# Kernel tuning notes

Measured on AMD Instinct MI355X. Metric: run time of the kernel, lower is better.

Reference implementation:

```python
import jax, jax.numpy as jnp
import numpy as np

NEG_SLOPE = 0.2
EPS = 1e-16


def setup_inputs() -> dict:
    N, E, IN, H, C = 100000, 1600000, 128, 4, 16
    key = jax.random.key(0)
    k1, k2, k3, k4, k5 = jax.random.split(key, 5)
    x = jax.random.normal(k1, (N, IN), dtype=jnp.float32)
    edge_index = jax.random.randint(k2, (2, E), 0, N, dtype=jnp.int64)
    # Xavier-uniform init like nn.init.xavier_uniform_
    limW = float(np.sqrt(6.0 / (IN + H * C)))
    W = jax.random.uniform(k3, (IN, H * C), dtype=jnp.float32, minval=-limW, maxval=limW)
    lima = float(np.sqrt(6.0 / (H + C)))
    att = jax.random.uniform(k4, (1, H, C), dtype=jnp.float32, minval=-lima, maxval=lima)
    bias = jnp.zeros((H * C,), dtype=jnp.float32)
    return {"x": x, "edge_index": edge_index, "W": W, "att": att, "bias": bias}


def reference(x, edge_index, W, att, bias):
    N = x.shape[0]
    H, C = att.shape[1], att.shape[2]
    h = (x @ W).reshape(N, H, C)  # [N,H,C]
    # add self loops
    loops = jnp.arange(N, dtype=edge_index.dtype)
    row = jnp.concatenate([edge_index[0], loops])  # target nodes
    col = jnp.concatenate([edge_index[1], loops])  # source nodes
    x_i = h[row]  # [Etot,H,C]
    x_j = h[col]
    e = jax.nn.leaky_relu(x_i + x_j, NEG_SLOPE)
    alpha = jnp.einsum('ehc,hc->eh', e, att[0])  # [Etot,H]
    # segment softmax keyed by row (every node has a self loop -> no empty segments)
    amax = jax.lax.stop_gradient(jax.ops.segment_max(alpha, row, num_segments=N))
    ea = jnp.exp(alpha - amax[row])
    denom = jax.ops.segment_sum(ea, row, num_segments=N)
    alpha = ea / (denom[row] + EPS)
    # weighted message scatter-add (dropout p=0 / eval mode)
    out = jax.ops.segment_sum(x_j * alpha[:, :, None], row, num_segments=N)  # [N,H,C]
    out = out.reshape(N, H * C) + bias  # concat=True
    return out
```

## Files before the change

### kernel.cpp

```cpp
#include <hip/hip_runtime.h>

#define NEG_SLOPE 0.2f

typedef float f32x4 __attribute__((ext_vector_type(4)));
typedef short bf16x8 __attribute__((ext_vector_type(8)));

__device__ __forceinline__ unsigned short f2bf(float f) {
  union { float f; unsigned u; } v; v.f = f;
  unsigned r = v.u + 0x7fff + ((v.u >> 16) & 1);
  return (unsigned short)(r >> 16);
}
__device__ __forceinline__ float bf2f(unsigned short u) {
  union { unsigned u; float f; } v; v.u = ((unsigned)u) << 16;
  return v.f;
}
__device__ __forceinline__ unsigned pkbf(float a, float b) {
  return (unsigned)f2bf(a) | ((unsigned)f2bf(b) << 16);
}
__device__ __forceinline__ f32x4 upk4(unsigned ux, unsigned uy) {
  union { unsigned u; float f; } a, b, c, d;
  a.u = ux << 16; b.u = ux & 0xffff0000u;
  c.u = uy << 16; d.u = uy & 0xffff0000u;
  f32x4 r; r.x = a.f; r.y = b.f; r.z = c.f; r.w = d.f;
  return r;
}
__device__ __forceinline__ f32x4 absfma(f32x4 s, f32x4 coef, f32x4 d) {
  d.x = fmaf(fabsf(s.x), coef.x, d.x);
  d.y = fmaf(fabsf(s.y), coef.y, d.y);
  d.z = fmaf(fabsf(s.z), coef.z, d.z);
  d.w = fmaf(fabsf(s.w), coef.w, d.w);
  return d;
}
__device__ __forceinline__ float dpp_xor1_add(float x) {
  int y = __builtin_amdgcn_mov_dpp(__builtin_bit_cast(int, x), 0xB1, 0xF, 0xF, true);
  return x + __builtin_bit_cast(float, y);
}
__device__ __forceinline__ float dpp_xor2_add(float x) {
  int y = __builtin_amdgcn_mov_dpp(__builtin_bit_cast(int, x), 0x4E, 0xF, 0xF, true);
  return x + __builtin_bit_cast(float, y);
}

#define TILE 4096
#define EPT 16
#define NBKT_MAX 256
#define SMEM_BYTES 24576

__device__ __forceinline__ void gemm_role(const float* __restrict__ x,
                                          const float* __restrict__ W,
                                          unsigned short* __restrict__ hb, int N,
                                          char* smem, int bid) {
  uint4* Bl = (uint4*)smem;
  const int t = threadIdx.x;
  {
    const int l = t & 63;
    const int kt = (t >> 6) & 3;
    const int kb = kt * 32 + ((l >> 4) * 8);
    const int cb = l & 15;
#pragma unroll
    for (int ct = 0; ct < 4; ct++) {
      const float* wp = W + (size_t)kb * 64 + ct * 16 + cb;
      unsigned p[4];
#pragma unroll
      for (int jj = 0; jj < 4; jj++)
        p[jj] = pkbf(wp[(2 * jj) * 64], wp[(2 * jj + 1) * 64]);
      Bl[(ct * 4 + kt) * 64 + l] = make_uint4(p[0], p[1], p[2], p[3]);
    }
  }
  __syncthreads();
  const int l = t & 63;
  const int wv = t >> 6;
  union BU { bf16x8 v; uint4 q; };
  BU b[4][4];
#pragma unroll
  for (int ct = 0; ct < 4; ct++)
#pragma unroll
    for (int kt = 0; kt < 4; kt++) b[ct][kt].q = Bl[(ct * 4 + kt) * 64 + l];

  const int rowbase0 = bid * 256 + wv * 64;
#pragma unroll
  for (int rt = 0; rt < 4; rt++) {
    const int rbase = rowbase0 + rt * 16;
    int rl = rbase + (l & 15);
    if (rl >= N) rl = N - 1;
    const float* xp = x + (size_t)rl * 128 + ((l >> 4) * 8);
    BU ah[4], alo[4];
#pragma unroll
    for (int kt = 0; kt < 4; kt++) {
      float f[8];
      float4 v0 = *(const float4*)(xp + kt * 32);
      float4 v1 = *(const float4*)(xp + kt * 32 + 4);
      f[0] = v0.x; f[1] = v0.y; f[2] = v0.z; f[3] = v0.w;
      f[4] = v1.x; f[5] = v1.y; f[6] = v1.z; f[7] = v1.w;
      unsigned short hs[8], ls[8];
#pragma unroll
      for (int j = 0; j < 8; j++) {
        hs[j] = f2bf(f[j]);
        ls[j] = f2bf(f[j] - bf2f(hs[j]));
      }
      ah[kt].q = make_uint4(hs[0] | (hs[1] << 16), hs[2] | (hs[3] << 16),
                            hs[4] | (hs[5] << 16), hs[6] | (hs[7] << 16));
      alo[kt].q = make_uint4(ls[0] | (ls[1] << 16), ls[2] | (ls[3] << 16),
                             ls[4] | (ls[5] << 16), ls[6] | (ls[7] << 16));
    }
#pragma unroll
    for (int ct = 0; ct < 4; ct++) {
      f32x4 acc = {0.f, 0.f, 0.f, 0.f};
#pragma unroll
      for (int kt = 0; kt < 4; kt++) {
        acc = __builtin_amdgcn_mfma_f32_16x16x32_bf16(ah[kt].v, b[ct][kt].v, acc, 0, 0, 0);
        acc = __builtin_amdgcn_mfma_f32_16x16x32_bf16(alo[kt].v, b[ct][kt].v, acc, 0, 0, 0);
      }
#pragma unroll
      for (int j = 0; j < 4; j++) {
        float v = acc[j];
        float pv = __shfl_xor(v, 1);
        int row = rbase + (l >> 4) * 4 + j;
        if (!(l & 1) && row < N) {
          *(unsigned*)((char*)hb + (size_t)row * 128 + ct * 32 + (l & 15) * 2) =
              pkbf(v, pv);
        }
      }
    }
  }
}

__device__ __forceinline__ void bucket_role(const int* __restrict__ rowi,
                                            const int* __restrict__ coli,
                                            int* __restrict__ bucket_fill,
                                            unsigned* __restrict__ bucket_arr, int E,
                                            int Cedge, int Ctot, int NBKT, char* smem,
                                            int bid) {
  int* cnt = (int*)smem;
  int* gadj = cnt + 256;
  int* tmp = gadj + 256;
  unsigned* staged = (unsigned*)(tmp + 256);
  unsigned char* bkof = (unsigned char*)(staged + TILE);
  const int t = threadIdx.x;
  const int tile0 = bid * TILE;
  const int nt = min(TILE, E - tile0);
  cnt[t] = 0;
  __syncthreads();
  unsigned pk[EPT];
  int bk[EPT];
#pragma unroll
  for (int j = 0; j < EPT; j++) {
    int i = tile0 + j * 256 + t;
    if (i < E) {
      int r = rowi[i];
      int c = coli[i];
      bk[j] = r >> 9;
      pk[j] = ((unsigned)(r & 511) << 17) | (unsigned)c;
      atomicAdd(&cnt[bk[j]], 1);
    } else {
      bk[j] = -1;
    }
  }
  __syncthreads();
  int v = cnt[t];
  tmp[t] = v;
  __syncthreads();
  for (int off = 1; off < 256; off <<= 1) {
    int val = tmp[t] + ((t >= off) ? tmp[t - off] : 0);
    __syncthreads();
    tmp[t] = val;
    __syncthreads();
  }
  int ex = tmp[t] - v;
  int ga = 0;
  if (v > 0) ga = atomicAdd(&bucket_fill[t], v);
  gadj[t] = ga - ex;
  cnt[t] = ex;
  __syncthreads();
#pragma unroll
  for (int j = 0; j < EPT; j++) {
    if (bk[j] >= 0) {
      int lp = atomicAdd(&cnt[bk[j]], 1);
      staged[lp] = pk[j];
      bkof[lp] = (unsigned char)bk[j];
    }
  }
  __syncthreads();
  for (int i = t; i < nt; i += 256) {
    int b = bkof[i];
    int pb = i + gadj[b];
    if (pb < Cedge) bucket_arr[b * Ctot + pb] = staged[i];
  }
}

__global__ __launch_bounds__(256) void gemm_bucket(const float* __restrict__ x,
                                                   const float* __restrict__ W,
                                                   unsigned short* __restrict__ hb, int N,
                                                   const int* __restrict__ rowi,
                                                   const int* __restrict__ coli,
                                                   int* __restrict__ bucket_fill,
                                                   unsigned* __restrict__ bucket_arr,
                                                   int E, int Cedge, int Ctot, int NBKT,
                                                   int G1) {
  __shared__ __align__(16) char smem[SMEM_BYTES];
  if ((int)blockIdx.x < G1)
    gemm_role(x, W, hb, N, smem, blockIdx.x);
  else
    bucket_role(rowi, coli, bucket_fill, bucket_arr, E, Cedge, Ctot, NBKT, smem,
                blockIdx.x - G1);
}

#define STAGE_CAP 10240

__global__ __launch_bounds__(1024) void csr_pass(unsigned* __restrict__ bucket_arr,
                                                 const int* __restrict__ bucket_fill,
                                                 int2* __restrict__ rowinfo,
                                                 int Cedge, int Ctot, int N) {
  __shared__ unsigned stage[STAGE_CAP];
  __shared__ int hist[512], excl[512], pairs[256];
  const int t = threadIdx.x;
  const int b = blockIdx.x;
  const int bb = b * Ctot;
  const int r0 = b << 9;
  const int nb = min(bucket_fill[b], Cedge);
  for (int i = t; i < 512; i += 1024) hist[i] = ((r0 + i) < N) ? 1 : 0;
  for (int i = t; i < nb; i += 1024) stage[i] = bucket_arr[bb + i];
  __syncthreads();
  for (int i = t; i < nb; i += 1024) atomicAdd(&hist[stage[i] >> 17], 1);
  __syncthreads();
  int h0 = 0, h1 = 0, ps = 0;
  if (t < 256) {
    h0 = hist[2 * t];
    h1 = hist[2 * t + 1];
    ps = h0 + h1;
    pairs[t] = ps;
  }
  __syncthreads();
  for (int off = 1; off < 256; off <<= 1) {
    int val = 0;
    if (t < 256) val = pairs[t] + ((t >= off) ? pairs[t - off] : 0);
    __syncthreads();
    if (t < 256) pairs[t] = val;
    __syncthreads();
  }
  if (t < 256) {
    int pexcl = pairs[t] - ps;
    excl[2 * t] = pexcl;
    excl[2 * t + 1] = pexcl + h0;
  }
  __syncthreads();
  for (int r = t; r < 512; r += 1024) {
    int gr = r0 + r;
    if (gr < N) {
      int o = bb + excl[r];
      rowinfo[gr] = make_int2(o, o + hist[r]);
    }
  }
  __syncthreads();
  for (int i = t; i < nb; i += 1024) {
    unsigned pk = stage[i];
    int r = pk >> 17;
    int lp = atomicAdd(&excl[r], 1);
    bucket_arr[bb + lp] = (pk & 0x1FFFFu) << 7;
  }
  __syncthreads();
  for (int r = t; r < 512; r += 1024) {
    int gr = r0 + r;
    if (gr < N) bucket_arr[bb + excl[r]] = (unsigned)gr << 7;
  }
}

#define ESTEPN(hivX, accX, denX, u)                     \
  {                                                     \
    f32x4 jv = upk4((u).x, (u).y);                      \
    f32x4 s = hivX + jv;                                \
    f32x4 d = s * attA;                                 \
    d = absfma(s, attB, d);                             \
    float al = (d.x + d.y) + (d.z + d.w);               \
    al = dpp_xor1_add(al);                              \
    al = dpp_xor2_add(al);                              \
    float p = exp2f(al);                                \
    accX += jv * p;                                     \
    denX += p;                                          \
  }

__global__ __launch_bounds__(256) void node_pass(const unsigned short* __restrict__ hb,
                                                 const int2* __restrict__ rowinfo,
                                                 const unsigned* __restrict__ srcs,
                                                 const float* __restrict__ att,
                                                 const float* __restrict__ bias,
                                                 float* __restrict__ out, int N) {
  const int wp = (blockIdx.x * blockDim.x + threadIdx.x) >> 6;
  const int a = wp * 2;
  if (a >= N) return;
  const bool bval = a + 1 < N;
  const int lane = threadIdx.x & 63;
  const int lr = lane & 15;
  const int q = lane >> 4;
  const char* hbc = (const char*)hb + (unsigned)(lr << 3);
  const unsigned* srcq = srcs + q;
  const f32x4 attv = *(const f32x4*)(att + 4 * lr);
  const f32x4 attA = attv * (0.6f * 1.44269504088896f);
  const f32x4 attB = attv * (0.4f * 1.44269504088896f);
  int4 ri;
  if (bval) {
    ri = *(const int4*)(rowinfo + a);
  } else {
    int2 t2 = rowinfo[a];
    ri = make_int4(t2.x, t2.y, t2.x, t2.x);
  }
  int ka = ri.x, kb = ri.z;
  const int ka1 = ri.y, kb1 = ri.w;
  uint2 hua = *(const uint2*)(hbc + ((size_t)a << 7));
  uint2 hub = *(const uint2*)(hbc + ((size_t)(bval ? a + 1 : a) << 7));
  const f32x4 hivA = upk4(hua.x, hua.y);
  const f32x4 hivB = upk4(hub.x, hub.y);
  f32x4 accA = {0.f, 0.f, 0.f, 0.f};
  f32x4 accB = {0.f, 0.f, 0.f, 0.f};
  float denA = 0.f, denB = 0.f;
  unsigned oa0, oa1, ob0, ob1;
  bool run = (ka + 8 <= ka1) & (kb + 8 <= kb1);
  if (run) {
    oa0 = srcq[ka];
    oa1 = srcq[ka + 4];
    ob0 = srcq[kb];
    ob1 = srcq[kb + 4];
  }
  while (run) {
    uint2 ua0 = *(const uint2*)(hbc + oa0);
    uint2 ua1 = *(const uint2*)(hbc + oa1);
    uint2 ub0 = *(const uint2*)(hbc + ob0);
    uint2 ub1 = *(const uint2*)(hbc + ob1);
    ka += 8;
    kb += 8;
    run = (ka + 8 <= ka1) & (kb + 8 <= kb1);
    if (run) {
      oa0 = srcq[ka];
      oa1 = srcq[ka + 4];
      ob0 = srcq[kb];
      ob1 = srcq[kb + 4];
    }
    ESTEPN(hivA, accA, denA, ua0);
    ESTEPN(hivA, accA, denA, ua1);
    ESTEPN(hivB, accB, denB, ub0);
    ESTEPN(hivB, accB, denB, ub1);
  }
  for (; ka + 8 <= ka1; ka += 8) {
    uint2 u0 = *(const uint2*)(hbc + srcq[ka]);
    uint2 u1 = *(const uint2*)(hbc + srcq[ka + 4]);
    ESTEPN(hivA, accA, denA, u0);
    ESTEPN(hivA, accA, denA, u1);
  }
  for (; kb + 8 <= kb1; kb += 8) {
    uint2 u0 = *(const uint2*)(hbc + srcq[kb]);
    uint2 u1 = *(const uint2*)(hbc + srcq[kb + 4]);
    ESTEPN(hivB, accB, denB, u0);
    ESTEPN(hivB, accB, denB, u1);
  }
  for (; ka + 4 <= ka1; ka += 4) {
    uint2 u = *(const uint2*)(hbc + srcq[ka]);
    ESTEPN(hivA, accA, denA, u);
  }
  for (; kb + 4 <= kb1; kb += 4) {
    uint2 u = *(const uint2*)(hbc + srcq[kb]);
    ESTEPN(hivB, accB, denB, u);
  }
  if (ka < ka1) {
    bool act = (ka + q) < ka1;
    uint2 u = *(const uint2*)(hbc + (act ? srcq[ka] : srcs[ka]));
    f32x4 jv = upk4(u.x, u.y);
    f32x4 s = hivA + jv;
    f32x4 d = s * attA;
    d = absfma(s, attB, d);
    float al = (d.x + d.y) + (d.z + d.w);
    al = dpp_xor1_add(al);
    al = dpp_xor2_add(al);
    float p = act ? exp2f(al) : 0.f;
    accA += jv * p;
    denA += p;
  }
  if (kb < kb1) {
    bool act = (kb + q) < kb1;
    uint2 u = *(const uint2*)(hbc + (act ? srcq[kb] : srcs[kb]));
    f32x4 jv = upk4(u.x, u.y);
    f32x4 s = hivB + jv;
    f32x4 d = s * attA;
    d = absfma(s, attB, d);
    float al = (d.x + d.y) + (d.z + d.w);
    al = dpp_xor1_add(al);
    al = dpp_xor2_add(al);
    float p = act ? exp2f(al) : 0.f;
    accB += jv * p;
    denB += p;
  }
#pragma unroll
  for (int j = 0; j < 4; j++) {
    accA[j] += __shfl_xor(accA[j], 16);
    accB[j] += __shfl_xor(accB[j], 16);
    accA[j] += __shfl_xor(accA[j], 32);
    accB[j] += __shfl_xor(accB[j], 32);
  }
  denA += __shfl_xor(denA, 16);
  denB += __shfl_xor(denB, 16);
  denA += __shfl_xor(denA, 32);
  denB += __shfl_xor(denB, 32);
  const f32x4 bv = *(const f32x4*)(bias + 4 * lr);
  if (q == 0) {
    float invA = 1.0f / (denA + 1e-16f);
    *(f32x4*)(out + (size_t)a * 64 + 4 * lr) = accA * invA + bv;
  } else if (q == 1 && bval) {
    float invB = 1.0f / (denB + 1e-16f);
    *(f32x4*)(out + (size_t)(a + 1) * 64 + 4 * lr) = accB * invB + bv;
  }
}

extern "C" void kernel_launch(void* const* d_in, const int* in_sizes, int n_in,
                              void* d_out, int out_size, void* d_ws, size_t ws_size,
                              hipStream_t stream) {
  const float* x = (const float*)d_in[0];
  const int* eidx = (const int*)d_in[1];
  const float* W = (const float*)d_in[2];
  const float* att = (const float*)d_in[3];
  const float* bias = (const float*)d_in[4];
  float* out = (float*)d_out;

  const int N = in_sizes[0] / 128;
  const int E = in_sizes[1] / 2;
  const int NBKT = (N + 511) >> 9;
  int Cedge = (E + NBKT - 1) / NBKT;
  Cedge = Cedge + Cedge / 8 + 64;
  Cedge = (Cedge + 15) & ~15;
  if (Cedge > STAGE_CAP) Cedge = STAGE_CAP;
  const int Ctot = Cedge + 512;

  unsigned short* hb = (unsigned short*)d_ws;
  int* bucket_fill = (int*)(hb + (size_t)N * 64);
  int2* rowinfo = (int2*)(bucket_fill + NBKT_MAX);
  unsigned* bucket_arr = (unsigned*)(rowinfo + N);

  hipMemsetAsync(bucket_fill, 0, NBKT_MAX * sizeof(int), stream);

  const int G1 = (N + 255) / 256;
  const int G2 = (E + TILE - 1) / TILE;
  gemm_bucket<<<G1 + G2, 256, 0, stream>>>(x, W, hb, N, eidx, eidx + E, bucket_fill,
                                           bucket_arr, E, Cedge, Ctot, NBKT, G1);
  csr_pass<<<NBKT, 1024, 0, stream>>>(bucket_arr, bucket_fill, rowinfo, Cedge, Ctot, N);
  const int npairs = (N + 1) / 2;
  node_pass<<<(npairs * 64 + 255) / 256, 256, 0, stream>>>(hb, rowinfo, bucket_arr, att,
                                                           bias, out, N);
}
```

Baseline: 103.6 us.

## Drop bf16 split-precision GEMM pass and simplify node_pass edge loop

```diff
diff --git a/kernel.cpp b/kernel.cpp
--- a/kernel.cpp
+++ b/kernel.cpp
@@ -9,10 +9,6 @@
   union { float f; unsigned u; } v; v.f = f;
   unsigned r = v.u + 0x7fff + ((v.u >> 16) & 1);
   return (unsigned short)(r >> 16);
-}
-__device__ __forceinline__ float bf2f(unsigned short u) {
-  union { unsigned u; float f; } v; v.u = ((unsigned)u) << 16;
-  return v.f;
 }
 __device__ __forceinline__ unsigned pkbf(float a, float b) {
   return (unsigned)f2bf(a) | ((unsigned)f2bf(b) << 16);
@@ -83,24 +79,13 @@
     int rl = rbase + (l & 15);
     if (rl >= N) rl = N - 1;
     const float* xp = x + (size_t)rl * 128 + ((l >> 4) * 8);
-    BU ah[4], alo[4];
+    BU ah[4];
 #pragma unroll
     for (int kt = 0; kt < 4; kt++) {
-      float f[8];
       float4 v0 = *(const float4*)(xp + kt * 32);
       float4 v1 = *(const float4*)(xp + kt * 32 + 4);
-      f[0] = v0.x; f[1] = v0.y; f[2] = v0.z; f[3] = v0.w;
-      f[4] = v1.x; f[5] = v1.y; f[6] = v1.z; f[7] = v1.w;
-      unsigned short hs[8], ls[8];
-#pragma unroll
-      for (int j = 0; j < 8; j++) {
-        hs[j] = f2bf(f[j]);
-        ls[j] = f2bf(f[j] - bf2f(hs[j]));
-      }
-      ah[kt].q = make_uint4(hs[0] | (hs[1] << 16), hs[2] | (hs[3] << 16),
-                            hs[4] | (hs[5] << 16), hs[6] | (hs[7] << 16));
-      alo[kt].q = make_uint4(ls[0] | (ls[1] << 16), ls[2] | (ls[3] << 16),
-                             ls[4] | (ls[5] << 16), ls[6] | (ls[7] << 16));
+      ah[kt].q = make_uint4(pkbf(v0.x, v0.y), pkbf(v0.z, v0.w),
+                            pkbf(v1.x, v1.y), pkbf(v1.z, v1.w));
     }
 #pragma unroll
     for (int ct = 0; ct < 4; ct++) {
@@ -108,7 +93,6 @@
 #pragma unroll
       for (int kt = 0; kt < 4; kt++) {
         acc = __builtin_amdgcn_mfma_f32_16x16x32_bf16(ah[kt].v, b[ct][kt].v, acc, 0, 0, 0);
-        acc = __builtin_amdgcn_mfma_f32_16x16x32_bf16(alo[kt].v, b[ct][kt].v, acc, 0, 0, 0);
       }
 #pragma unroll
       for (int j = 0; j < 4; j++) {
@@ -287,7 +271,9 @@
   const int wp = (blockIdx.x * blockDim.x + threadIdx.x) >> 6;
   const int a = wp * 2;
   if (a >= N) return;
-  const bool bval = a + 1 < N;
+  const int bn = a + 1;
+  const bool bval = bn < N;
+  const int bc = bval ? bn : a;
   const int lane = threadIdx.x & 63;
   const int lr = lane & 15;
   const int q = lane >> 4;
@@ -296,48 +282,29 @@
   const f32x4 attv = *(const f32x4*)(att + 4 * lr);
   const f32x4 attA = attv * (0.6f * 1.44269504088896f);
   const f32x4 attB = attv * (0.4f * 1.44269504088896f);
-  int4 ri;
-  if (bval) {
-    ri = *(const int4*)(rowinfo + a);
-  } else {
-    int2 t2 = rowinfo[a];
-    ri = make_int4(t2.x, t2.y, t2.x, t2.x);
-  }
-  int ka = ri.x, kb = ri.z;
-  const int ka1 = ri.y, kb1 = ri.w;
+  const int2 ria = rowinfo[a];
+  const int2 rib = rowinfo[bc];
   uint2 hua = *(const uint2*)(hbc + ((size_t)a << 7));
-  uint2 hub = *(const uint2*)(hbc + ((size_t)(bval ? a + 1 : a) << 7));
+  uint2 hub = *(const uint2*)(hbc + ((size_t)bc << 7));
   const f32x4 hivA = upk4(hua.x, hua.y);
   const f32x4 hivB = upk4(hub.x, hub.y);
+  int ka = ria.x, kb = rib.x;
+  const int ka1 = ria.y;
+  const int kb1 = bval ? rib.y : rib.x;
   f32x4 accA = {0.f, 0.f, 0.f, 0.f};
   f32x4 accB = {0.f, 0.f, 0.f, 0.f};
   float denA = 0.f, denB = 0.f;
-  unsigned oa0, oa1, ob0, ob1;
-  bool run = (ka + 8 <= ka1) & (kb + 8 <= kb1);
-  if (run) {
-    oa0 = srcq[ka];
-    oa1 = srcq[ka + 4];
-    ob0 = srcq[kb];
-    ob1 = srcq[kb + 4];
-  }
-  while (run) {
-    uint2 ua0 = *(const uint2*)(hbc + oa0);
-    uint2 ua1 = *(const uint2*)(hbc + oa1);
-    uint2 ub0 = *(const uint2*)(hbc + ob0);
-    uint2 ub1 = *(const uint2*)(hbc + ob1);
-    ka += 8;
-    kb += 8;
-    run = (ka + 8 <= ka1) & (kb + 8 <= kb1);
-    if (run) {
-      oa0 = srcq[ka];
-      oa1 = srcq[ka + 4];
-      ob0 = srcq[kb];
-      ob1 = srcq[kb + 4];
-    }
+  while (ka + 8 <= ka1 && kb + 8 <= kb1) {
+    uint2 ua0 = *(const uint2*)(hbc + srcq[ka]);
+    uint2 ua1 = *(const uint2*)(hbc + srcq[ka + 4]);
+    uint2 ub0 = *(const uint2*)(hbc + srcq[kb]);
+    uint2 ub1 = *(const uint2*)(hbc + srcq[kb + 4]);
     ESTEPN(hivA, accA, denA, ua0);
     ESTEPN(hivA, accA, denA, ua1);
     ESTEPN(hivB, accB, denB, ub0);
     ESTEPN(hivB, accB, denB, ub1);
+    ka += 8;
+    kb += 8;
   }
   for (; ka + 8 <= ka1; ka += 8) {
     uint2 u0 = *(const uint2*)(hbc + srcq[ka]);
@@ -398,13 +365,14 @@
   denB += __shfl_xor(denB, 16);
   denA += __shfl_xor(denA, 32);
   denB += __shfl_xor(denB, 32);
-  const f32x4 bv = *(const f32x4*)(bias + 4 * lr);
   if (q == 0) {
+    const f32x4 bv = *(const f32x4*)(bias + 4 * lr);
     float invA = 1.0f / (denA + 1e-16f);
     *(f32x4*)(out + (size_t)a * 64 + 4 * lr) = accA * invA + bv;
-  } else if (q == 1 && bval) {
-    float invB = 1.0f / (denB + 1e-16f);
-    *(f32x4*)(out + (size_t)(a + 1) * 64 + 4 * lr) = accB * invB + bv;
+    if (bval) {
+      float invB = 1.0f / (denB + 1e-16f);
+      *(f32x4*)(out + (size_t)bn * 64 + 4 * lr) = accB * invB + bv;
+    }
   }
 }
 
@@ -439,7 +407,6 @@
   gemm_bucket<<<G1 + G2, 256, 0, stream>>>(x, W, hb, N, eidx, eidx + E, bucket_fill,
                                            bucket_arr, E, Cedge, Ctot, NBKT, G1);
   csr_pass<<<NBKT, 1024, 0, stream>>>(bucket_arr, bucket_fill, rowinfo, Cedge, Ctot, N);
-  const int npairs = (N + 1) / 2;
-  node_pass<<<(npairs * 64 + 255) / 256, 256, 0, stream>>>(hb, rowinfo, bucket_arr, att,
-                                                           bias, out, N);
-}
+  node_pass<<<(N * 32 + 255) / 256, 256, 0, stream>>>(hb, rowinfo, bucket_arr, att, bias,
+                                                      out, N);
+}
```

Measured after the change: 97.21 us. 6.2% less time.
